# Optimization experiments

Measured on AMD Instinct MI355X. Metric: run time of the kernel, lower is better.

The kernel has to match this reference:

```python
import jax, jax.numpy as jnp
import numpy as np

D, DEPTH, HEADS, P, IMG = 768, 12, 12, 16, 224
GRID = IMG // P
NTOK = GRID * GRID + 1  # 197
PLEN, NTASK, NCLS = 5, 5, 100
DEEP = (2, 3, 4)
HD = D // HEADS
LN_EPS = 1e-6


def _ln(x, w, b):
    m = x.mean(-1, keepdims=True)
    v = ((x - m) ** 2).mean(-1, keepdims=True)
    return (x - m) * jax.lax.rsqrt(v + LN_EPS) * w + b


def _l2n(x):
    return x * jax.lax.rsqrt(jnp.maximum((x * x).sum(-1, keepdims=True), 1e-12))


def _mlp(x, w1, b1, w2, b2):
    return jax.nn.gelu(x @ w1.T + b1, approximate=False) @ w2.T + b2


def _mha(x, wqkv, bqkv, wp, bp):
    B, N, _ = x.shape
    qkv = (x @ wqkv.T + bqkv).reshape(B, N, 3, HEADS, HD)
    q, k, v = qkv[:, :, 0], qkv[:, :, 1], qkv[:, :, 2]
    a = jax.nn.softmax(jnp.einsum('bnhd,bmhd->bhnm', q * HD ** -0.5, k), -1)
    o = jnp.einsum('bhnm,bmhd->bnhd', a, v).reshape(B, N, D)
    return o @ wp.T + bp


def _block(x, i, p):
    x = x + _mha(_ln(x, p['ln1_w'][i], p['ln1_b'][i]), p['qkv_w'][i], p['qkv_b'][i], p['proj_w'][i], p['proj_b'][i])
    return x + _mlp(_ln(x, p['ln2_w'][i], p['ln2_b'][i]), p['fc1_w'][i], p['fc1_b'][i], p['fc2_w'][i], p['fc2_b'][i])


def _blocks(x, p):
    for i in range(DEPTH):
        x = _block(x, i, p)
    return x


def _deep_block(x, i, li, prompts, p):
    # single-head prefix-prompt attention exactly as written in the torch module,
    # including the (buggy but faithful) transpose(1,2).reshape(B,N,C) scramble
    B, N, _ = x.shape
    nx = _ln(x, p['ln1_w'][i], p['ln1_b'][i])
    qkv = (nx @ p['qkv_w'][i].T + p['qkv_b'][i]).reshape(B, N, 3, D)
    q, k, v = qkv[:, :, 0], qkv[:, :, 1], qkv[:, :, 2]
    k = jnp.concatenate([prompts[:, 2 * li], k], axis=1)
    v = jnp.concatenate([prompts[:, 2 * li + 1], v], axis=1)
    a = jax.nn.softmax(jnp.einsum('bnd,bmd->bnm', q, k) * HD ** -0.5, -1)
    av = jnp.einsum('bnm,bmd->bnd', a, v)
    av = av.swapaxes(1, 2).reshape(B, N, D)
    x = x + (av @ p['proj_w'][i].T + p['proj_b'][i])
    return x + _mlp(_ln(x, p['ln2_w'][i], p['ln2_b'][i]), p['fc1_w'][i], p['fc1_b'][i], p['fc2_w'][i], p['fc2_b'][i])


def _embed(inputs, patch_w, patch_b, cls_token, pos_embed):
    B = inputs.shape[0]
    x = inputs.reshape(B, 3, GRID, P, GRID, P).transpose(0, 2, 4, 1, 3, 5).reshape(B, GRID * GRID, 3 * P * P)
    x = x @ patch_w.T + patch_b
    x = jnp.concatenate([jnp.broadcast_to(cls_token, (B, 1, D)), x], axis=1)
    return x + pos_embed


def _branch_forward(x, sel_main, main_idx, sub_idx, p, main_prompts, sub_prompt, pos_embed, fc_w, fc_b, norm_w, norm_b):
    B = x.shape[0]
    # ---- main branch: per-sample gathered deep prompts ----
    mx = x[main_idx]
    mp = main_prompts[sel_main].reshape(mx.shape[0], 2 * len(DEEP), PLEN, D)
    for i in range(DEPTH):
        if i in DEEP:
            mx = _deep_block(mx, i, DEEP.index(i), mp, p)
        else:
            mx = _block(mx, i, p)
    mx = _ln(mx, norm_w, norm_b)
    mlog = mx[:, 0] @ fc_w.T + fc_b  # fc_norm is Identity in timm vit_base
    # ---- sub branch: prepend sub prompts after cls ----
    sx = x[sub_idx]
    sp = jnp.broadcast_to(sub_prompt[0] + pos_embed[0, 0], (sx.shape[0], PLEN, D))
    sx = jnp.concatenate([sx[:, :1], sp, sx[:, 1:]], axis=1)
    sx = _ln(_blocks(sx, p), norm_w, norm_b)
    slog = sx[:, 1:1 + PLEN].mean(axis=1) @ fc_w.T + fc_b
    # scatter back to per-sample logits (fixed output shape)
    return jnp.zeros((B, NCLS), x.dtype).at[main_idx].set(mlog).at[sub_idx].set(slog)


def setup_inputs() -> dict:
    key = jax.random.key(0)
    ks = iter(jax.random.split(key, 32))
    nk = lambda: next(ks)
    r = lambda shape, sc=0.02: jax.random.normal(nk(), shape, jnp.float32) * sc
    return {
        'inputs': jax.random.normal(nk(), (16, 3, IMG, IMG), jnp.float32),
        'task_id': 4,
        'patch_w': r((D, 3 * P * P)),
        'patch_b': jnp.zeros((D,)),
        'cls_token': r((1, 1, D)),
        'pos_embed': r((1, NTOK, D)),
        'qkv_w': r((DEPTH, 3 * D, D)),
        'qkv_b': jnp.zeros((DEPTH, 3 * D)),
        'proj_w': r((DEPTH, D, D)),
        'proj_b': jnp.zeros((DEPTH, D)),
        'ln1_w': jnp.ones((DEPTH, D)), 'ln1_b': jnp.zeros((DEPTH, D)),
        'ln2_w': jnp.ones((DEPTH, D)), 'ln2_b': jnp.zeros((DEPTH, D)),
        'fc1_w': r((DEPTH, 4 * D, D)),
        'fc1_b': jnp.zeros((DEPTH, 4 * D)),
        'fc2_w': r((DEPTH, D, 4 * D)),
        'fc2_b': jnp.zeros((DEPTH, D)),
        'norm_w': jnp.ones((D,)), 'norm_b': jnp.zeros((D,)),
        'fc_w': r((NCLS, D)),
        'fc_b': jnp.zeros((NCLS,)),
        'main_key': r((NTASK, D), 1.0),
        'sub_key': r((1, D), 1.0),
        'main_prompts': r((NTASK, 1, 2, len(DEEP), PLEN, D), 1.0),
        'sub_prompt': r((1, PLEN, D), 1.0),
    }


def reference(inputs, task_id, patch_w, patch_b, cls_token, pos_embed, qkv_w, qkv_b, proj_w, proj_b,
              ln1_w, ln1_b, ln2_w, ln2_b, fc1_w, fc1_b, fc2_w, fc2_b, norm_w, norm_b, fc_w, fc_b,
              main_key, sub_key, main_prompts, sub_prompt):
    p = dict(qkv_w=qkv_w, qkv_b=qkv_b, proj_w=proj_w, proj_b=proj_b, ln1_w=ln1_w, ln1_b=ln1_b,
             ln2_w=ln2_w, ln2_b=ln2_b, fc1_w=fc1_w, fc1_b=fc1_b, fc2_w=fc2_w, fc2_b=fc2_b)
    x = _embed(inputs, patch_w, patch_b, cls_token, pos_embed)
    # frozen query pass (torch.no_grad in the original)
    query = _ln(_blocks(x, p), norm_w, norm_b)[:, 0]
    # test-time routing: cosine similarity to [main_key[:task_id+1], sub_key]
    cand = jnp.concatenate([main_key[:task_id + 1], sub_key], axis=0)
    sim = _l2n(query) @ _l2n(cand).T
    sel = jnp.argmax(sim, axis=1)  # selection_size == 1
    main_mask = sel <= task_id
    main_idx = jnp.nonzero(main_mask)[0]
    sub_idx = jnp.nonzero(jnp.logical_not(main_mask))[0]
    sel_main = sel[main_idx]
    return _branch_forward(x, sel_main, main_idx, sub_idx, p, main_prompts, sub_prompt, pos_embed,
                           fc_w, fc_b, norm_w, norm_b)
```

## Files before the change

kernel.cpp:

```cpp
#include <hip/hip_runtime.h>
#include <math.h>

#define B_    16
#define NT_   197
#define NS_   202
#define HEADS_ 12
#define DEPTH_ 12
#define NCLS_ 100
#define MROW_ (B_ * NT_)
#define SROW_ (B_ * NS_)
#define CROW_ (MROW_ + SROW_)
#define PAD_  128
#define TAILC_ 96
#define TAILM_ 16

typedef __attribute__((ext_vector_type(8))) short short8v;
typedef __attribute__((ext_vector_type(4))) float f32x4;

__device__ __forceinline__ short f2bf(float f){
    unsigned u = __builtin_bit_cast(unsigned, f);
    unsigned r = (u + 0x7FFFu + ((u >> 16) & 1u)) >> 16;
    return (short)r;
}
__device__ __forceinline__ unsigned pk2(float a, float b){
    return (unsigned)(unsigned short)f2bf(a) | (((unsigned)(unsigned short)f2bf(b)) << 16);
}
__device__ __forceinline__ float bf2f(unsigned short s){
    unsigned u = ((unsigned)s) << 16;
    return __builtin_bit_cast(float, u);
}
__device__ __forceinline__ float4 ld4bf(const short* p){
    uint2 u = *(const uint2*)p;
    float4 r;
    r.x = bf2f((unsigned short)(u.x & 0xffff));
    r.y = bf2f((unsigned short)(u.x >> 16));
    r.z = bf2f((unsigned short)(u.y & 0xffff));
    r.w = bf2f((unsigned short)(u.y >> 16));
    return r;
}
__device__ __forceinline__ void gld16(const short* g, short* l){
    __builtin_amdgcn_global_load_lds(
        (const __attribute__((address_space(1))) unsigned*)g,
        (__attribute__((address_space(3))) unsigned*)l, 16, 0, 0);
}

__device__ __forceinline__ double block_reduce_sum_d(double s, double* red, int lane, int wid){
#pragma unroll
    for (int off = 32; off; off >>= 1) s += __shfl_xor(s, off);
    if (lane == 0) red[wid] = s;
    __syncthreads();
    double S = red[0] + red[1] + red[2] + red[3];
    __syncthreads();
    return S;
}

__global__ void convert_w_k(const float* __restrict__ in, short* __restrict__ out, long n){
    long i = ((long)blockIdx.x * 256 + threadIdx.x) * 8;
    long stride = (long)gridDim.x * 256 * 8;
    for (; i < n; i += stride){
        float4 a = *(const float4*)(in + i);
        float4 b = *(const float4*)(in + i + 4);
        uint4 o4;
        o4.x = pk2(a.x, a.y); o4.y = pk2(a.z, a.w);
        o4.z = pk2(b.x, b.y); o4.w = pk2(b.z, b.w);
        *(uint4*)(out + i) = o4;
    }
}

template<int EPI, int WB>
__global__ __launch_bounds__(256) void gemm_bf16(
    const short* __restrict__ A, const void* __restrict__ Wv,
    const float* __restrict__ bias, const float* __restrict__ Res,
    float* __restrict__ Cf, short* __restrict__ Cb, int M, int K, int N)
{
    __shared__ short As0[128 * 32];
    __shared__ short As1[128 * 32];
    __shared__ short Bs0[128 * 32];
    __shared__ short Bs1[128 * 32];
    const int t = threadIdx.x;
    const int lane = t & 63, wid = t >> 6;
    const int wr = wid >> 1, wc = wid & 1;
    const long row0 = (long)blockIdx.y * 128;
    const long col0 = (long)blockIdx.x * 128;

    f32x4 acc[4][4];
#pragma unroll
    for (int i = 0; i < 4; i++)
#pragma unroll
        for (int j = 0; j < 4; j++) acc[i][j] = (f32x4){0.f, 0.f, 0.f, 0.f};

    const int l15 = lane & 15, lkg = lane >> 4;
    const int lrow = lane >> 2;
    const int lcol = (lane & 3) * 8;

    for (int k0 = 0; k0 < K; k0 += 64){
#pragma unroll
        for (int i = 0; i < 2; i++){
            int rb = wid * 32 + i * 16;
            const short* gs = A + (row0 + rb + lrow) * K + k0 + lcol;
            gld16(gs,      &As0[rb * 32]);
            gld16(gs + 32, &As1[rb * 32]);
        }
        if (WB == 1){
            const short* Wb = (const short*)Wv;
#pragma unroll
            for (int i = 0; i < 2; i++){
                int rb = wid * 32 + i * 16;
                const short* gs = Wb + (col0 + rb + lrow) * K + k0 + lcol;
                gld16(gs,      &Bs0[rb * 32]);
                gld16(gs + 32, &Bs1[rb * 32]);
            }
        } else {
            const float* Wf = (const float*)Wv;
            const int bn = t >> 1, bh = t & 1;
#pragma unroll
            for (int half = 0; half < 2; half++){
                const float* Wp = Wf + (col0 + bn) * K + k0 + half * 32 + bh * 16;
                unsigned rr[8];
#pragma unroll
                for (int g = 0; g < 8; g++){
                    float2 f = *(const float2*)(Wp + g * 2);
                    rr[g] = pk2(f.x, f.y);
                }
                uint4 lo = {rr[0], rr[1], rr[2], rr[3]};
                uint4 hi = {rr[4], rr[5], rr[6], rr[7]};
                short* Bsh = half ? Bs1 : Bs0;
                *(uint4*)(&Bsh[bn * 32 + bh * 16])     = lo;
                *(uint4*)(&Bsh[bn * 32 + bh * 16 + 8]) = hi;
            }
        }
        __syncthreads();

        {
            short8v a[4], b[4];
#pragma unroll
            for (int i = 0; i < 4; i++)
                a[i] = *(const short8v*)(&As0[(wr * 64 + i * 16 + l15) * 32 + lkg * 8]);
#pragma unroll
            for (int j = 0; j < 4; j++)
                b[j] = *(const short8v*)(&Bs0[(wc * 64 + j * 16 + l15) * 32 + lkg * 8]);
#pragma unroll
            for (int i = 0; i < 4; i++)
#pragma unroll
                for (int j = 0; j < 4; j++)
                    acc[i][j] = __builtin_amdgcn_mfma_f32_16x16x32_bf16(a[i], b[j], acc[i][j], 0, 0, 0);
        }
        {
            short8v a[4], b[4];
#pragma unroll
            for (int i = 0; i < 4; i++)
                a[i] = *(const short8v*)(&As1[(wr * 64 + i * 16 + l15) * 32 + lkg * 8]);
#pragma unroll
            for (int j = 0; j < 4; j++)
                b[j] = *(const short8v*)(&Bs1[(wc * 64 + j * 16 + l15) * 32 + lkg * 8]);
#pragma unroll
            for (int i = 0; i < 4; i++)
#pragma unroll
                for (int j = 0; j < 4; j++)
                    acc[i][j] = __builtin_amdgcn_mfma_f32_16x16x32_bf16(a[i], b[j], acc[i][j], 0, 0, 0);
        }
        __syncthreads();
    }

#pragma unroll
    for (int i = 0; i < 4; i++){
#pragma unroll
        for (int q = 0; q < 4; q++){
            long gr = row0 + wr * 64 + i * 16 + lkg * 4 + q;
            if (gr >= M) continue;
#pragma unroll
            for (int j = 0; j < 4; j++){
                long gc = col0 + wc * 64 + j * 16 + l15;
                float v = acc[i][j][q] + bias[gc];
                if (EPI == 1){
                    v = 0.5f * v * (1.f + erff(v * 0.70710678118654752f));
                    Cb[gr * N + gc] = f2bf(v);
                } else if (EPI == 2){
                    Cf[gr * N + gc] = v + Res[gr * N + gc];
                } else if (EPI == 3){
                    Cb[gr * N + gc] = f2bf(v);
                } else {
                    Cf[gr * N + gc] = v;
                }
            }
        }
    }
}

__global__ __launch_bounds__(256) void ln_k(const float* __restrict__ x,
    const float* __restrict__ w, const float* __restrict__ b,
    short* __restrict__ y, int M)
{
    const int lane = threadIdx.x & 63, wv = threadIdx.x >> 6;
    const int row = blockIdx.x * 4 + wv;
    if (row >= M) return;
    const float* xr = x + (long)row * 768;
    float v[12];
    float s = 0.f;
#pragma unroll
    for (int j = 0; j < 12; j++){ v[j] = xr[lane + j * 64]; s += v[j]; }
#pragma unroll
    for (int off = 32; off; off >>= 1) s += __shfl_xor(s, off);
    float m = s * (1.f / 768.f);
    float q = 0.f;
#pragma unroll
    for (int j = 0; j < 12; j++){ v[j] -= m; q += v[j] * v[j]; }
#pragma unroll
    for (int off = 32; off; off >>= 1) q += __shfl_xor(q, off);
    float rs = 1.f / sqrtf(q * (1.f / 768.f) + 1e-6f);
    short* yr = y + (long)row * 768;
#pragma unroll
    for (int j = 0; j < 12; j++)
        yr[lane + j * 64] = f2bf(v[j] * rs * w[lane + j * 64] + b[lane + j * 64]);
}

__global__ __launch_bounds__(512) void attn_mfma(
    const short* __restrict__ qkv0, short* __restrict__ o0, int N0, int tb0, int te0,
    const short* __restrict__ qkv1, short* __restrict__ o1, int N1, int tb1, int te1)
{
    __shared__ short Ks[208 * 72];
    __shared__ short Vs[64 * 232];
    __shared__ short Ps[8 * 16 * 40];
    const int bh = blockIdx.x;
    const int b = bh / HEADS_, h = bh % HEADS_;
    const int seg = blockIdx.y;
    const short* qkv = seg ? qkv1 : qkv0;
    short* o = seg ? o1 : o0;
    const int Ntok = seg ? N1 : N0;
    const int tb = seg ? tb1 : tb0;
    const int te = seg ? te1 : te0;
    const int t = threadIdx.x, lane = t & 63, wid = t >> 6;
    const long rb = (long)b * Ntok;

    {
        const int r = t >> 2, c = (t & 3) * 16;
#pragma unroll
        for (int pass = 0; pass < 2; pass++){
            int m = r + pass * 128;
            if (m < 208){
                if (m < Ntok){
                    const short* kr = qkv + (rb + m) * 2304 + 768  + h * 64 + c;
                    const short* vr = qkv + (rb + m) * 2304 + 1536 + h * 64 + c;
                    *(uint4*)(&Ks[m * 72 + c])     = *(const uint4*)(kr);
                    *(uint4*)(&Ks[m * 72 + c + 8]) = *(const uint4*)(kr + 8);
#pragma unroll
                    for (int j = 0; j < 16; j++)
                        Vs[(c + j) * 232 + m] = vr[j];
                } else {
#pragma unroll
                    for (int j = 0; j < 16; j += 2)
                        *(unsigned*)(&Ks[m * 72 + c + j]) = 0u;
#pragma unroll
                    for (int j = 0; j < 16; j++)
                        Vs[(c + j) * 232 + m] = 0;
                }
            }
        }
        for (int i = t; i < 64 * 16; i += 512){
            int d = i >> 4, m = 208 + (i & 15);
            Vs[d * 232 + m] = 0;
        }
    }
    __syncthreads();

    const int l15 = lane & 15, lkg = lane >> 4;
    short* Pw = &Ps[wid * 16 * 40];

    for (int s = tb + wid; s < te; s += 8){
        const int q0 = s * 16;
        short8v a0, a1;
        {
            int qrow = q0 + l15;
            if (qrow < Ntok){
                const short* qp = qkv + (rb + qrow) * 2304 + h * 64;
                a0 = *(const short8v*)(qp + lkg * 8);
                a1 = *(const short8v*)(qp + 32 + lkg * 8);
            } else {
                uint4 z = {0u,0u,0u,0u};
                a0 = __builtin_bit_cast(short8v, z);
                a1 = __builtin_bit_cast(short8v, z);
            }
        }
        f32x4 sacc[13];
#pragma unroll
        for (int j = 0; j < 13; j++){
            short8v b0 = *(const short8v*)(&Ks[(j * 16 + l15) * 72 + lkg * 8]);
            short8v b1 = *(const short8v*)(&Ks[(j * 16 + l15) * 72 + 32 + lkg * 8]);
            f32x4 z = {0.f, 0.f, 0.f, 0.f};
            z = __builtin_amdgcn_mfma_f32_16x16x32_bf16(a0, b0, z, 0, 0, 0);
            z = __builtin_amdgcn_mfma_f32_16x16x32_bf16(a1, b1, z, 0, 0, 0);
            sacc[j][0] = z[0] * 0.125f; sacc[j][1] = z[1] * 0.125f;
            sacc[j][2] = z[2] * 0.125f; sacc[j][3] = z[3] * 0.125f;
        }
#pragma unroll
        for (int j = 0; j < 13; j++){
            if (j * 16 + l15 >= Ntok){
                sacc[j][0] = -1e30f; sacc[j][1] = -1e30f;
                sacc[j][2] = -1e30f; sacc[j][3] = -1e30f;
            }
        }
#pragma unroll
        for (int rr = 0; rr < 4; rr++){
            float mx = sacc[0][rr];
#pragma unroll
            for (int j = 1; j < 13; j++) mx = fmaxf(mx, sacc[j][rr]);
            mx = fmaxf(mx, __shfl_xor(mx, 1));
            mx = fmaxf(mx, __shfl_xor(mx, 2));
            mx = fmaxf(mx, __shfl_xor(mx, 4));
            mx = fmaxf(mx, __shfl_xor(mx, 8));
            float pv[13];
            float sum = 0.f;
#pragma unroll
            for (int j = 0; j < 13; j++){
                float e = expf(sacc[j][rr] - mx);
                pv[j] = e; sum += e;
            }
            sum += __shfl_xor(sum, 1);
            sum += __shfl_xor(sum, 2);
            sum += __shfl_xor(sum, 4);
            sum += __shfl_xor(sum, 8);
            float inv = 1.f / sum;
#pragma unroll
            for (int j = 0; j < 13; j++) sacc[j][rr] = pv[j] * inv;
        }
        f32x4 oacc[4];
#pragma unroll
        for (int dj = 0; dj < 4; dj++) oacc[dj] = (f32x4){0.f, 0.f, 0.f, 0.f};
#pragma unroll
        for (int kc = 0; kc < 7; kc++){
            const int j0 = 2 * kc, j1 = 2 * kc + 1;
#pragma unroll
            for (int rr = 0; rr < 4; rr++){
                Pw[(lkg * 4 + rr) * 40 + l15]      = f2bf(sacc[j0][rr]);
                Pw[(lkg * 4 + rr) * 40 + 16 + l15] = (j1 < 13) ? f2bf(sacc[j1][rr]) : (short)0;
            }
            short8v pa = *(const short8v*)(&Pw[l15 * 40 + lkg * 8]);
#pragma unroll
            for (int dj = 0; dj < 4; dj++){
                short8v vb = *(const short8v*)(&Vs[(dj * 16 + l15) * 232 + kc * 32 + lkg * 8]);
                oacc[dj] = __builtin_amdgcn_mfma_f32_16x16x32_bf16(pa, vb, oacc[dj], 0, 0, 0);
            }
        }
#pragma unroll
        for (int dj = 0; dj < 4; dj++){
#pragma unroll
            for (int rr = 0; rr < 4; rr++){
                int q = q0 + lkg * 4 + rr;
                if (q < Ntok)
                    o[(rb + q) * 768 + h * 64 + dj * 16 + l15] = f2bf(oacc[dj][rr]);
            }
        }
    }
}

__global__ __launch_bounds__(512) void attn_deep_v4(
    const short* __restrict__ qkv, const float* __restrict__ prompts,
    const int* __restrict__ selm, short* __restrict__ o, int li)
{
    __shared__ float sc[4][208];
    __shared__ float part[12][256];
    const int b = blockIdx.x, g = blockIdx.y, t = threadIdx.x;
    const int lane = t & 63, w = t >> 6;
    const int n0 = g * 4;

    float4 q0[4], q1[4], q2[4];
#pragma unroll
    for (int qi = 0; qi < 4; qi++){
        int n = n0 + qi;
        int nn = (n < NT_) ? n : (NT_ - 1);
        const short* qr = qkv + (long)(b * NT_ + nn) * 2304;
        q0[qi] = ld4bf(qr + lane * 4);
        q1[qi] = ld4bf(qr + 256 + lane * 4);
        q2[qi] = ld4bf(qr + 512 + lane * 4);
    }

    const float* kp = prompts + ((long)selm[b] * 6 + 2 * li) * 5 * 768;
    const float* vp = kp + 5 * 768;

    for (int m = w; m < 202; m += 8){
        float4 k0, k1, k2;
        if (m < 5){
            const float* kr = kp + (long)m * 768;
            k0 = *(const float4*)(kr + lane * 4);
            k1 = *(const float4*)(kr + 256 + lane * 4);
            k2 = *(const float4*)(kr + 512 + lane * 4);
        } else {
            const short* kr = qkv + (long)(b * NT_ + (m - 5)) * 2304 + 768;
            k0 = ld4bf(kr + lane * 4);
            k1 = ld4bf(kr + 256 + lane * 4);
            k2 = ld4bf(kr + 512 + lane * 4);
        }
        float a[4];
#pragma unroll
        for (int qi = 0; qi < 4; qi++){
            a[qi] = q0[qi].x*k0.x + q0[qi].y*k0.y + q0[qi].z*k0.z + q0[qi].w*k0.w
                  + q1[qi].x*k1.x + q1[qi].y*k1.y + q1[qi].z*k1.z + q1[qi].w*k1.w
                  + q2[qi].x*k2.x + q2[qi].y*k2.y + q2[qi].z*k2.z + q2[qi].w*k2.w;
        }
#pragma unroll
        for (int off = 32; off; off >>= 1){
#pragma unroll
            for (int qi = 0; qi < 4; qi++) a[qi] += __shfl_xor(a[qi], off);
        }
        if (lane == 0){
#pragma unroll
            for (int qi = 0; qi < 4; qi++) sc[qi][m] = a[qi] * 0.125f;
        }
    }
    __syncthreads();

    if (w < 4){
        float v[4];
#pragma unroll
        for (int i = 0; i < 4; i++){
            int m = lane + i * 64;
            v[i] = (m < 202) ? sc[w][m] : -1e30f;
        }
        float mx = fmaxf(fmaxf(v[0], v[1]), fmaxf(v[2], v[3]));
#pragma unroll
        for (int off = 32; off; off >>= 1) mx = fmaxf(mx, __shfl_xor(mx, off));
        float e[4], sum = 0.f;
#pragma unroll
        for (int i = 0; i < 4; i++){
            int m = lane + i * 64;
            e[i] = (m < 202) ? expf(v[i] - mx) : 0.f;
            sum += e[i];
        }
#pragma unroll
        for (int off = 32; off; off >>= 1) sum += __shfl_xor(sum, off);
        float inv = 1.f / sum;
#pragma unroll
        for (int i = 0; i < 4; i++){
            int m = lane + i * 64;
            if (m < 202) sc[w][m] = e[i] * inv;
        }
    }
    __syncthreads();

    const int grp = t >> 8;
    const int tt = t & 255;
    float a0[4] = {0.f,0.f,0.f,0.f}, a1[4] = {0.f,0.f,0.f,0.f}, a2[4] = {0.f,0.f,0.f,0.f};
    if (grp == 0){
        for (int m = 0; m < 5; m++){
            const float* vr = vp + (long)m * 768;
            float v0 = vr[tt], v1 = vr[tt + 256], v2 = vr[tt + 512];
#pragma unroll
            for (int qi = 0; qi < 4; qi++){
                float pm = sc[qi][m];
                a0[qi] += pm * v0; a1[qi] += pm * v1; a2[qi] += pm * v2;
            }
        }
        for (int m = 5; m < 103; m++){
            const short* vr = qkv + (long)(b * NT_ + (m - 5)) * 2304 + 1536;
            float v0 = bf2f((unsigned short)vr[tt]);
            float v1 = bf2f((unsigned short)vr[tt + 256]);
            float v2 = bf2f((unsigned short)vr[tt + 512]);
#pragma unroll
            for (int qi = 0; qi < 4; qi++){
                float pm = sc[qi][m];
                a0[qi] += pm * v0; a1[qi] += pm * v1; a2[qi] += pm * v2;
            }
        }
    } else {
        for (int m = 103; m < 202; m++){
            const short* vr = qkv + (long)(b * NT_ + (m - 5)) * 2304 + 1536;
            float v0 = bf2f((unsigned short)vr[tt]);
            float v1 = bf2f((unsigned short)vr[tt + 256]);
            float v2 = bf2f((unsigned short)vr[tt + 512]);
#pragma unroll
            for (int qi = 0; qi < 4; qi++){
                float pm = sc[qi][m];
                a0[qi] += pm * v0; a1[qi] += pm * v1; a2[qi] += pm * v2;
            }
        }
#pragma unroll
        for (int qi = 0; qi < 4; qi++){
            part[qi * 3 + 0][tt] = a0[qi];
            part[qi * 3 + 1][tt] = a1[qi];
            part[qi * 3 + 2][tt] = a2[qi];
        }
    }
    __syncthreads();
    if (grp == 0){
#pragma unroll
        for (int qi = 0; qi < 4; qi++){
            float f0 = a0[qi] + part[qi * 3 + 0][tt];
            float f1 = a1[qi] + part[qi * 3 + 1][tt];
            float f2 = a2[qi] + part[qi * 3 + 2][tt];
            int n = n0 + qi;
            if (n < NT_){
                short* ob = o + (long)b * NT_ * 768 + n;
                ob[(long)tt * 197]         = f2bf(f0);
                ob[(long)(tt + 256) * 197] = f2bf(f1);
                ob[(long)(tt + 512) * 197] = f2bf(f2);
            }
        }
    }
}

__device__ __forceinline__ long tail_src_row(int r, int mode){
    if (mode == 1) return (long)r * NT_;
    if (r < 16)    return (long)r * NT_;
    int j = r - 16;
    return (long)MROW_ + (long)(j / 5) * NS_ + 1 + (j % 5);
}
__global__ void gather_tail_f(const float* __restrict__ src, float* __restrict__ dst,
                              int nrows, int mode){
    long i = (long)blockIdx.x * 256 + threadIdx.x;
    long total = (long)nrows * 768;
    if (i >= total) return;
    int r = (int)(i / 768), d = (int)(i % 768);
    dst[i] = src[tail_src_row(r, mode) * 768 + d];
}
__global__ void gather_tail_b(const short* __restrict__ src, short* __restrict__ dst,
                              int nrows, int mode){
    long i = (long)blockIdx.x * 256 + threadIdx.x;
    long total = (long)nrows * 768;
    if (i >= total) return;
    int r = (int)(i / 768), d = (int)(i % 768);
    dst[i] = src[tail_src_row(r, mode) * 768 + d];
}

__global__ void unfold_k(const float* __restrict__ in, short* __restrict__ out){
    long i = (long)blockIdx.x * 256 + threadIdx.x;
    long total = (long)B_ * 196 * 768;
    if (i >= total) return;
    int f = (int)(i % 768); long rw = i / 768;
    int t = (int)(rw % 196); int b = (int)(rw / 196);
    int gy = t / 14, gx = t % 14;
    int c = f >> 8, rem = f & 255, py = rem >> 4, px = rem & 15;
    out[i] = f2bf(in[(((long)(b * 3 + c) * 224) + gy * 16 + py) * 224 + gx * 16 + px]);
}

__global__ void assemble_k(const float* __restrict__ pe, const float* __restrict__ cls,
    const float* __restrict__ pos, float* __restrict__ x0){
    long i = (long)blockIdx.x * 256 + threadIdx.x;
    long total = (long)B_ * NT_ * 768;
    if (i >= total) return;
    int d = (int)(i % 768); long rw = i / 768;
    int n = (int)(rw % NT_); int b = (int)(rw / NT_);
    float v;
    if (n == 0) v = cls[d] + pos[d];
    else        v = pe[((long)b * 196 + (n - 1)) * 768 + d] + pos[(long)n * 768 + d];
    x0[i] = v;
}

__global__ void copy_f(const float* __restrict__ a, float* __restrict__ b, long total){
    long i = (long)blockIdx.x * 256 + threadIdx.x;
    if (i < total) b[i] = a[i];
}

__global__ void build_sub_k(const float* __restrict__ x0, const float* __restrict__ subp,
    const float* __restrict__ pos, float* __restrict__ xSub){
    long i = (long)blockIdx.x * 256 + threadIdx.x;
    long total = (long)B_ * NS_ * 768;
    if (i >= total) return;
    int d = (int)(i % 768); long rw = i / 768;
    int n = (int)(rw % NS_); int b = (int)(rw / NS_);
    float v;
    if (n == 0)      v = x0[((long)b * NT_) * 768 + d];
    else if (n <= 5) v = subp[(n - 1) * 768 + d] + pos[d];
    else             v = x0[((long)b * NT_ + (n - 5)) * 768 + d];
    xSub[i] = v;
}

__global__ __launch_bounds__(256) void select_k(
    const float* __restrict__ xT, const float* __restrict__ norm_w,
    const float* __restrict__ norm_b, const float* __restrict__ main_key,
    const float* __restrict__ sub_key, const int* __restrict__ task_id_p,
    int* __restrict__ selm, int* __restrict__ flag)
{
    __shared__ double red[4];
    int b = blockIdx.x, t = threadIdx.x, lane = t & 63, wid = t >> 6;
    const float* xr = xT + (long)b * 768;
    double v0 = xr[t], v1 = xr[t + 256], v2 = xr[t + 512];
    double S = block_reduce_sum_d(v0 + v1 + v2, red, lane, wid);
    double m = S * (1.0 / 768.0);
    double d0 = v0 - m, d1 = v1 - m, d2 = v2 - m;
    double Q = block_reduce_sum_d(d0*d0 + d1*d1 + d2*d2, red, lane, wid);
    double rs = 1.0 / sqrt(Q * (1.0 / 768.0) + 1e-6);
    double q0 = d0 * rs * (double)norm_w[t]       + (double)norm_b[t];
    double q1 = d1 * rs * (double)norm_w[t + 256] + (double)norm_b[t + 256];
    double q2 = d2 * rs * (double)norm_w[t + 512] + (double)norm_b[t + 512];
    double qn = block_reduce_sum_d(q0*q0 + q1*q1 + q2*q2, red, lane, wid);
    double qinv = 1.0 / sqrt(fmax(qn, 1e-12));

    int tk = *task_id_p;
    int ncand = tk + 2;
    double best = -1e300; int bsel = 0;
    for (int c = 0; c < ncand; c++){
        const float* cr = (c <= tk) ? (main_key + (long)c * 768) : sub_key;
        double c0 = cr[t], c1 = cr[t + 256], c2 = cr[t + 512];
        double dotq = block_reduce_sum_d(q0*c0 + q1*c1 + q2*c2, red, lane, wid);
        double nc   = block_reduce_sum_d(c0*c0 + c1*c1 + c2*c2, red, lane, wid);
        double sim = dotq * qinv * (1.0 / sqrt(fmax(nc, 1e-12)));
        if (sim > best){ best = sim; bsel = c; }
    }
    if (t == 0){
        int isMain = (bsel <= tk) ? 1 : 0;
        selm[b] = isMain ? bsel : 0;
        flag[b] = isMain;
    }
}

__global__ __launch_bounds__(256) void head_k(
    const float* __restrict__ xMT, const float* __restrict__ xT,
    const float* __restrict__ norm_w, const float* __restrict__ norm_b,
    const float* __restrict__ fc_w, const float* __restrict__ fc_b,
    const int* __restrict__ flag, float* __restrict__ out)
{
    __shared__ double vec[768];
    __shared__ double red[4];
    int b = blockIdx.x, t = threadIdx.x, lane = t & 63, wid = t >> 6;
    int isMain = flag[b];
    double a0 = 0.0, a1 = 0.0, a2 = 0.0;
    int nrows = isMain ? 1 : 5;
    for (int rI = 0; rI < nrows; rI++){
        const float* xr = isMain ? (xMT + (long)b * 768)
                                 : (xT + (long)(16 + b * 5 + rI) * 768);
        double v0 = xr[t], v1 = xr[t + 256], v2 = xr[t + 512];
        double S = block_reduce_sum_d(v0 + v1 + v2, red, lane, wid);
        double m = S * (1.0 / 768.0);
        double d0 = v0 - m, d1 = v1 - m, d2 = v2 - m;
        double Q = block_reduce_sum_d(d0*d0 + d1*d1 + d2*d2, red, lane, wid);
        double rs = 1.0 / sqrt(Q * (1.0 / 768.0) + 1e-6);
        a0 += d0 * rs * (double)norm_w[t]       + (double)norm_b[t];
        a1 += d1 * rs * (double)norm_w[t + 256] + (double)norm_b[t + 256];
        a2 += d2 * rs * (double)norm_w[t + 512] + (double)norm_b[t + 512];
    }
    double scl = isMain ? 1.0 : 0.2;
    vec[t] = a0 * scl; vec[t + 256] = a1 * scl; vec[t + 512] = a2 * scl;
    __syncthreads();
    if (t < NCLS_){
        const float* wr = fc_w + (long)t * 768;
        double acc = (double)fc_b[t];
#pragma unroll 8
        for (int j = 0; j < 768; j++) acc += vec[j] * (double)wr[j];
        out[b * NCLS_ + t] = (float)acc;
    }
}

struct Params {
    const float *qkv_w, *qkv_b, *proj_w, *proj_b;
    const float *ln1_w, *ln1_b, *ln2_w, *ln2_b;
    const float *fc1_w, *fc1_b, *fc2_w, *fc2_b;
    const float *prompts; const int* selm;
    short *lnb, *attb, *hidb;
    short *qkvb;
    const short *qkv_wc, *proj_wc, *fc1_wc, *fc2_wc;
    bool cache;
    float *xT, *xMT;
    short *attbT, *lnbT, *hidT;
};

template<int EPI>
static void launch_gemm(hipStream_t st, const short* A, const float* Wf, const short* Wc,
                        bool cache, const float* bias, const float* Res,
                        float* Cf, short* Cb, int M, int K, int N)
{
    dim3 g(N / 128, (M + 127) / 128);
    if (cache)
        gemm_bf16<EPI, 1><<<g, 256, 0, st>>>(A, (const void*)Wc, bias, Res, Cf, Cb, M, K, N);
    else
        gemm_bf16<EPI, 0><<<g, 256, 0, st>>>(A, (const void*)Wf, bias, Res, Cf, Cb, M, K, N);
}

static void run_layer(hipStream_t st, float* x, int M, int layer, int mode, int li,
                      const Params& P)
{
    int lnGrid = (M + 3) / 4;
    ln_k<<<lnGrid, 256, 0, st>>>(x, P.ln1_w + layer * 768, P.ln1_b + layer * 768, P.lnb, M);
    launch_gemm<3>(st, P.lnb, P.qkv_w + (long)layer * 2304 * 768,
        P.qkv_wc + (P.cache ? (long)layer * 2304 * 768 : 0), P.cache,
        P.qkv_b + layer * 2304, nullptr, nullptr, P.qkvb, M, 768, 2304);
    if (mode == 0){
        attn_mfma<<<dim3(B_ * HEADS_, 2), 512, 0, st>>>(
            P.qkvb, P.attb, NT_, 0, 13,
            P.qkvb + (long)MROW_ * 2304, P.attb + (long)MROW_ * 768, NS_, 0, 13);
    } else if (mode == 1){
        attn_mfma<<<dim3(B_ * HEADS_, 2), 512, 0, st>>>(
            P.qkvb, P.attb, NT_, 0, 7,
            P.qkvb, P.attb, NT_, 7, 13);
    } else {
        attn_deep_v4<<<dim3(B_, 50), 512, 0, st>>>(P.qkvb, P.prompts, P.selm, P.attb, li);
    }
    launch_gemm<2>(st, P.attb, P.proj_w + (long)layer * 768 * 768,
        P.proj_wc + (P.cache ? (long)layer * 768 * 768 : 0), P.cache,
        P.proj_b + layer * 768, x, x, nullptr, M, 768, 768);
    ln_k<<<lnGrid, 256, 0, st>>>(x, P.ln2_w + layer * 768, P.ln2_b + layer * 768, P.lnb, M);
    launch_gemm<1>(st, P.lnb, P.fc1_w + (long)layer * 3072 * 768,
        P.fc1_wc + (P.cache ? (long)layer * 3072 * 768 : 0), P.cache,
        P.fc1_b + layer * 3072, nullptr, nullptr, P.hidb, M, 768, 3072);
    launch_gemm<2>(st, P.hidb, P.fc2_w + (long)layer * 768 * 3072,
        P.fc2_wc + (P.cache ? (long)layer * 768 * 3072 : 0), P.cache,
        P.fc2_b + layer * 768, x, x, nullptr, M, 3072, 768);
}

static void run_layer_tail(hipStream_t st, float* x, int M, int layer, int gmode,
                           const Params& P)
{
    int lnGrid = (M + 3) / 4;
    ln_k<<<lnGrid, 256, 0, st>>>(x, P.ln1_w + layer * 768, P.ln1_b + layer * 768, P.lnb, M);
    launch_gemm<3>(st, P.lnb, P.qkv_w + (long)layer * 2304 * 768,
        P.qkv_wc + (P.cache ? (long)layer * 2304 * 768 : 0), P.cache,
        P.qkv_b + layer * 2304, nullptr, nullptr, P.qkvb, M, 768, 2304);
    if (gmode == 0){
        attn_mfma<<<dim3(B_ * HEADS_, 2), 512, 0, st>>>(
            P.qkvb, P.attb, NT_, 0, 1,
            P.qkvb + (long)MROW_ * 2304, P.attb + (long)MROW_ * 768, NS_, 0, 1);
    } else {
        attn_mfma<<<dim3(B_ * HEADS_, 1), 512, 0, st>>>(
            P.qkvb, P.attb, NT_, 0, 1,
            P.qkvb, P.attb, NT_, 0, 1);
    }
    const int Mt = (gmode == 0) ? TAILC_ : TAILM_;
    float* xt = (gmode == 0) ? P.xT : P.xMT;
    long tot = (long)Mt * 768;
    gather_tail_f<<<(int)((tot + 255) / 256), 256, 0, st>>>(x, xt, Mt, gmode);
    gather_tail_b<<<(int)((tot + 255) / 256), 256, 0, st>>>(P.attb, P.attbT, Mt, gmode);
    launch_gemm<2>(st, P.attbT, P.proj_w + (long)layer * 768 * 768,
        P.proj_wc + (P.cache ? (long)layer * 768 * 768 : 0), P.cache,
        P.proj_b + layer * 768, xt, xt, nullptr, Mt, 768, 768);
    ln_k<<<(Mt + 3) / 4, 256, 0, st>>>(xt, P.ln2_w + layer * 768, P.ln2_b + layer * 768,
                                       P.lnbT, Mt);
    launch_gemm<1>(st, P.lnbT, P.fc1_w + (long)layer * 3072 * 768,
        P.fc1_wc + (P.cache ? (long)layer * 3072 * 768 : 0), P.cache,
        P.fc1_b + layer * 3072, nullptr, nullptr, P.hidT, Mt, 768, 3072);
    launch_gemm<2>(st, P.hidT, P.fc2_w + (long)layer * 768 * 3072,
        P.fc2_wc + (P.cache ? (long)layer * 768 * 3072 : 0), P.cache,
        P.fc2_b + layer * 768, xt, xt, nullptr, Mt, 3072, 768);
}

extern "C" void kernel_launch(void* const* d_in, const int* in_sizes, int n_in,
                              void* d_out, int out_size, void* d_ws, size_t ws_size,
                              hipStream_t stream)
{
    (void)in_sizes; (void)n_in; (void)out_size;
    const float* inputs   = (const float*)d_in[0];
    const int*   task_id  = (const int*)  d_in[1];
    const float* patch_w  = (const float*)d_in[2];
    const float* patch_b  = (const float*)d_in[3];
    const float* cls_tok  = (const float*)d_in[4];
    const float* pos      = (const float*)d_in[5];
    const float* qkv_w    = (const float*)d_in[6];
    const float* qkv_b    = (const float*)d_in[7];
    const float* proj_w   = (const float*)d_in[8];
    const float* proj_b   = (const float*)d_in[9];
    const float* ln1_w    = (const float*)d_in[10];
    const float* ln1_b    = (const float*)d_in[11];
    const float* ln2_w    = (const float*)d_in[12];
    const float* ln2_b    = (const float*)d_in[13];
    const float* fc1_w    = (const float*)d_in[14];
    const float* fc1_b    = (const float*)d_in[15];
    const float* fc2_w    = (const float*)d_in[16];
    const float* fc2_b    = (const float*)d_in[17];
    const float* norm_w   = (const float*)d_in[18];
    const float* norm_b   = (const float*)d_in[19];
    const float* fc_w     = (const float*)d_in[20];
    const float* fc_b     = (const float*)d_in[21];
    const float* main_key = (const float*)d_in[22];
    const float* sub_key  = (const float*)d_in[23];
    const float* m_prompts= (const float*)d_in[24];
    const float* s_prompt = (const float*)d_in[25];
    float* out = (float*)d_out;

    char* wsb = (char*)d_ws;
    size_t off = 0;
    auto allocB = [&](size_t bytes) -> void* {
        void* p = (void*)(wsb + off);
        off += (bytes + 255) & ~(size_t)255;
        return p;
    };
    float* xC   = (float*)allocB((size_t)CROW_ * 768 * 4);
    float* xM   = (float*)allocB((size_t)MROW_ * 768 * 4);
    short* lnb  = (short*)allocB((size_t)(CROW_ + PAD_) * 768 * 2);
    short* attb = (short*)allocB((size_t)(CROW_ + PAD_) * 768 * 2);
    short* qkvb = (short*)allocB((size_t)(CROW_ + PAD_) * 2304 * 2);
    short* hidb = (short*)allocB((size_t)(CROW_ + PAD_) * 3072 * 2);
    float* peo  = (float*)allocB((size_t)3136 * 768 * 4);
    float* xT    = (float*)allocB((size_t)TAILC_ * 768 * 4);
    float* xMT   = (float*)allocB((size_t)TAILM_ * 768 * 4);
    short* attbT = (short*)allocB((size_t)(TAILC_ + PAD_) * 768 * 2);
    short* lnbT  = (short*)allocB((size_t)(TAILC_ + PAD_) * 768 * 2);
    short* hidT  = (short*)allocB((size_t)(TAILC_ + PAD_) * 3072 * 2);
    int*   selm = (int*)allocB(64);
    int*   flag = (int*)allocB(64);

    const size_t nQkv = (size_t)DEPTH_ * 2304 * 768;
    const size_t nProj = (size_t)DEPTH_ * 768 * 768;
    const size_t nFc1 = (size_t)DEPTH_ * 3072 * 768;
    const size_t nFc2 = (size_t)DEPTH_ * 768 * 3072;
    const size_t nPatch = (size_t)768 * 768;
    size_t cacheBytes = (nQkv + nProj + nFc1 + nFc2 + nPatch) * 2 + 5 * 256;
    bool cache = (ws_size >= off + cacheBytes + (1u << 20));
    short *qkv_wc = nullptr, *proj_wc = nullptr, *fc1_wc = nullptr, *fc2_wc = nullptr, *patch_wc = nullptr;
    if (cache){
        qkv_wc  = (short*)allocB(nQkv * 2);
        proj_wc = (short*)allocB(nProj * 2);
        fc1_wc  = (short*)allocB(nFc1 * 2);
        fc2_wc  = (short*)allocB(nFc2 * 2);
        patch_wc= (short*)allocB(nPatch * 2);
        convert_w_k<<<2048, 256, 0, stream>>>(qkv_w,  qkv_wc,  (long)nQkv);
        convert_w_k<<<1024, 256, 0, stream>>>(proj_w, proj_wc, (long)nProj);
        convert_w_k<<<2048, 256, 0, stream>>>(fc1_w,  fc1_wc,  (long)nFc1);
        convert_w_k<<<2048, 256, 0, stream>>>(fc2_w,  fc2_wc,  (long)nFc2);
        convert_w_k<<<256,  256, 0, stream>>>(patch_w, patch_wc, (long)nPatch);
    }

    Params P;
    P.qkv_w = qkv_w; P.qkv_b = qkv_b; P.proj_w = proj_w; P.proj_b = proj_b;
    P.ln1_w = ln1_w; P.ln1_b = ln1_b; P.ln2_w = ln2_w; P.ln2_b = ln2_b;
    P.fc1_w = fc1_w; P.fc1_b = fc1_b; P.fc2_w = fc2_w; P.fc2_b = fc2_b;
    P.prompts = m_prompts; P.selm = selm;
    P.lnb = lnb; P.attb = attb; P.hidb = hidb; P.qkvb = qkvb;
    P.qkv_wc = qkv_wc; P.proj_wc = proj_wc; P.fc1_wc = fc1_wc; P.fc2_wc = fc2_wc;
    P.cache = cache;
    P.xT = xT; P.xMT = xMT; P.attbT = attbT; P.lnbT = lnbT; P.hidT = hidT;

    const long XN = (long)MROW_ * 768;

    {
        long tot = (long)B_ * 196 * 768;
        short* un = hidb;
        unfold_k<<<(int)((tot + 255) / 256), 256, 0, stream>>>(inputs, un);
        launch_gemm<0>(stream, un, patch_w, patch_wc, cache, patch_b, nullptr,
                       peo, nullptr, 3136, 768, 768);
        assemble_k<<<(int)((XN + 255) / 256), 256, 0, stream>>>(peo, cls_tok, pos, xC);
        long st = (long)SROW_ * 768;
        build_sub_k<<<(int)((st + 255) / 256), 256, 0, stream>>>(xC, s_prompt, pos,
                                                                 xC + (long)MROW_ * 768);
    }

    for (int i = 0; i < DEPTH_ - 1; i++){
        run_layer(stream, xC, CROW_, i, 0, 0, P);
        if (i == 1)
            copy_f<<<(int)((XN + 255) / 256), 256, 0, stream>>>(xC, xM, XN);
    }
    run_layer_tail(stream, xC, CROW_, DEPTH_ - 1, 0, P);

    select_k<<<16, 256, 0, stream>>>(xT, norm_w, norm_b, main_key, sub_key,
                                     task_id, selm, flag);

    for (int i = 2; i < DEPTH_ - 1; i++){
        int mode = (i >= 2 && i <= 4) ? 2 : 1;
        run_layer(stream, xM, MROW_, i, mode, i - 2, P);
    }
    run_layer_tail(stream, xM, MROW_, DEPTH_ - 1, 1, P);

    head_k<<<16, 256, 0, stream>>>(xMT, xT, norm_w, norm_b, fc_w, fc_b, flag, out);
}
```

Before: 5.219 ms.

## Double-buffer bf16 GEMM K-loop to overlap global loads with MFMA

The bf16-weight GEMM path now uses a ping-pong pair of LDS buffers with a K step of 32. It issues the global-to-LDS loads for the next K slice before running the MFMAs on the current slice, which cuts the per-iteration syncs from two to one and hides load latency. The fp32-weight path is rewritten to step K by 32 with a single buffer, so it does twice as many iterations and barriers. The risk is less work per barrier and whether the async gld16 writes have landed before the sync.

New measurement: 5.482 ms. +5.0%, slower.

```diff
diff --git a/kernel.cpp b/kernel.cpp
--- a/kernel.cpp
+++ b/kernel.cpp
@@ -73,10 +73,8 @@
     const float* __restrict__ bias, const float* __restrict__ Res,
     float* __restrict__ Cf, short* __restrict__ Cb, int M, int K, int N)
 {
-    __shared__ short As0[128 * 32];
-    __shared__ short As1[128 * 32];
-    __shared__ short Bs0[128 * 32];
-    __shared__ short Bs1[128 * 32];
+    __shared__ short As[2][128 * 32];
+    __shared__ short Bs[2][128 * 32];
     const int t = threadIdx.x;
     const int lane = t & 63, wid = t >> 6;
     const int wr = wid >> 1, wc = wid & 1;
@@ -93,29 +91,51 @@
     const int lrow = lane >> 2;
     const int lcol = (lane & 3) * 8;
 
-    for (int k0 = 0; k0 < K; k0 += 64){
+    if (WB == 1){
+        const short* Wb = (const short*)Wv;
 #pragma unroll
         for (int i = 0; i < 2; i++){
             int rb = wid * 32 + i * 16;
-            const short* gs = A + (row0 + rb + lrow) * K + k0 + lcol;
-            gld16(gs,      &As0[rb * 32]);
-            gld16(gs + 32, &As1[rb * 32]);
-        }
-        if (WB == 1){
-            const short* Wb = (const short*)Wv;
+            gld16(A  + (row0 + rb + lrow) * K + lcol, &As[0][rb * 32]);
+            gld16(Wb + (col0 + rb + lrow) * K + lcol, &Bs[0][rb * 32]);
+        }
+        __syncthreads();
+        int cur = 0;
+        for (int k0 = 0; k0 < K; k0 += 32){
+            if (k0 + 32 < K){
+#pragma unroll
+                for (int i = 0; i < 2; i++){
+                    int rb = wid * 32 + i * 16;
+                    gld16(A  + (row0 + rb + lrow) * K + k0 + 32 + lcol, &As[cur ^ 1][rb * 32]);
+                    gld16(Wb + (col0 + rb + lrow) * K + k0 + 32 + lcol, &Bs[cur ^ 1][rb * 32]);
+                }
+            }
+            short8v a[4], b[4];
+#pragma unroll
+            for (int i = 0; i < 4; i++)
+                a[i] = *(const short8v*)(&As[cur][(wr * 64 + i * 16 + l15) * 32 + lkg * 8]);
+#pragma unroll
+            for (int j = 0; j < 4; j++)
+                b[j] = *(const short8v*)(&Bs[cur][(wc * 64 + j * 16 + l15) * 32 + lkg * 8]);
+#pragma unroll
+            for (int i = 0; i < 4; i++)
+#pragma unroll
+                for (int j = 0; j < 4; j++)
+                    acc[i][j] = __builtin_amdgcn_mfma_f32_16x16x32_bf16(a[i], b[j], acc[i][j], 0, 0, 0);
+            __syncthreads();
+            cur ^= 1;
+        }
+    } else {
+        const float* Wf = (const float*)Wv;
+        const int bn = t >> 1, bh = t & 1;
+        for (int k0 = 0; k0 < K; k0 += 32){
 #pragma unroll
             for (int i = 0; i < 2; i++){
                 int rb = wid * 32 + i * 16;
-                const short* gs = Wb + (col0 + rb + lrow) * K + k0 + lcol;
-                gld16(gs,      &Bs0[rb * 32]);
-                gld16(gs + 32, &Bs1[rb * 32]);
-            }
-        } else {
-            const float* Wf = (const float*)Wv;
-            const int bn = t >> 1, bh = t & 1;
-#pragma unroll
-            for (int half = 0; half < 2; half++){
-                const float* Wp = Wf + (col0 + bn) * K + k0 + half * 32 + bh * 16;
+                gld16(A + (row0 + rb + lrow) * K + k0 + lcol, &As[0][rb * 32]);
+            }
+            {
+                const float* Wp = Wf + (col0 + bn) * K + k0 + bh * 16;
                 unsigned rr[8];
 #pragma unroll
                 for (int g = 0; g < 8; g++){
@@ -124,42 +144,24 @@
                 }
                 uint4 lo = {rr[0], rr[1], rr[2], rr[3]};
                 uint4 hi = {rr[4], rr[5], rr[6], rr[7]};
-                short* Bsh = half ? Bs1 : Bs0;
-                *(uint4*)(&Bsh[bn * 32 + bh * 16])     = lo;
-                *(uint4*)(&Bsh[bn * 32 + bh * 16 + 8]) = hi;
-            }
-        }
-        __syncthreads();
-
-        {
+                *(uint4*)(&Bs[0][bn * 32 + bh * 16])     = lo;
+                *(uint4*)(&Bs[0][bn * 32 + bh * 16 + 8]) = hi;
+            }
+            __syncthreads();
             short8v a[4], b[4];
 #pragma unroll
             for (int i = 0; i < 4; i++)
-                a[i] = *(const short8v*)(&As0[(wr * 64 + i * 16 + l15) * 32 + lkg * 8]);
+                a[i] = *(const short8v*)(&As[0][(wr * 64 + i * 16 + l15) * 32 + lkg * 8]);
 #pragma unroll
             for (int j = 0; j < 4; j++)
-                b[j] = *(const short8v*)(&Bs0[(wc * 64 + j * 16 + l15) * 32 + lkg * 8]);
+                b[j] = *(const short8v*)(&Bs[0][(wc * 64 + j * 16 + l15) * 32 + lkg * 8]);
 #pragma unroll
             for (int i = 0; i < 4; i++)
 #pragma unroll
                 for (int j = 0; j < 4; j++)
                     acc[i][j] = __builtin_amdgcn_mfma_f32_16x16x32_bf16(a[i], b[j], acc[i][j], 0, 0, 0);
-        }
-        {
-            short8v a[4], b[4];
-#pragma unroll
-            for (int i = 0; i < 4; i++)
-                a[i] = *(const short8v*)(&As1[(wr * 64 + i * 16 + l15) * 32 + lkg * 8]);
-#pragma unroll
-            for (int j = 0; j < 4; j++)
-                b[j] = *(const short8v*)(&Bs1[(wc * 64 + j * 16 + l15) * 32 + lkg * 8]);
-#pragma unroll
-            for (int i = 0; i < 4; i++)
-#pragma unroll
-                for (int j = 0; j < 4; j++)
-                    acc[i][j] = __builtin_amdgcn_mfma_f32_16x16x32_bf16(a[i], b[j], acc[i][j], 0, 0, 0);
-        }
-        __syncthreads();
+            __syncthreads();
+        }
     }
 
 #pragma unroll
```
